# Kernel tuning notes

Measured on AMD Instinct MI355X. Metric: run time of the kernel, lower is better.

The kernel has to match this reference:

```python
import jax, jax.numpy as jnp
import numpy as np

B, C, W, H = 4, 128, 64, 64
CK = 32  # f/g projection channels


def setup_inputs() -> dict:
    key = jax.random.key(0)
    ks = jax.random.split(key, 8)
    s_in = 1.0 / np.sqrt(C)
    return {
        "x": jax.random.normal(ks[0], (B, C, W, H), dtype=jnp.float32),
        "Wf": jax.random.normal(ks[1], (CK, C), dtype=jnp.float32) * s_in,
        "bf": jnp.zeros((CK,), dtype=jnp.float32),
        "Wg": jax.random.normal(ks[2], (CK, C), dtype=jnp.float32) * s_in,
        "bg": jnp.zeros((CK,), dtype=jnp.float32),
        "Wh": jax.random.normal(ks[3], (C, C), dtype=jnp.float32) * s_in,
        "bh": jnp.zeros((C,), dtype=jnp.float32),
        "gamma": jax.random.normal(ks[4], (1,), dtype=jnp.float32) * 0.1,
    }


def reference(x, Wf, bf, Wg, bg, Wh, bh, gamma):
    b, c, w, h = x.shape
    n = w * h
    xf = x.reshape(b, c, n)                                  # [B,C,N]
    # 1x1 convs == per-pixel linear projections
    f = jnp.einsum('oc,bcn->bon', Wf, xf) + bf[None, :, None]  # [B,32,N]
    g = jnp.einsum('oc,bcn->bon', Wg, xf) + bg[None, :, None]  # [B,32,N]
    v = jnp.einsum('oc,bcn->bon', Wh, xf) + bh[None, :, None]  # [B,C,N]
    # attention = softmax(f^T g) over last dim (g positions), as in the torch code
    att = jax.nn.softmax(jnp.einsum('bkn,bkm->bnm', f, g), axis=-1)  # [B,N,N]
    # self_attention = h @ attention  (contract over f-position axis)
    sa = jnp.einsum('bcn,bnm->bcm', v, att).reshape(b, c, w, h)
    return gamma[0] * sa + x
```

## Files before the change

### kernel.cpp

```cpp
#include <hip/hip_runtime.h>
#include <hip/hip_bf16.h>

#define BB 4
#define CC 128
#define NN 4096
#define CK 32
#define L2E 1.442695040888963f

typedef __attribute__((ext_vector_type(8))) short short8v;
typedef __attribute__((ext_vector_type(4))) float float4v;

__device__ inline ushort f2bf(float f) {
    union { __hip_bfloat16 h; ushort u; } cv;
    cv.h = __float2bfloat16(f);
    return cv.u;
}
__device__ inline float bf2f(ushort u) {
    union { uint u; float f; } cv;
    cv.u = ((uint)u) << 16;
    return cv.f;
}
__device__ inline uint pk2(float lo, float hi) {
    return ((uint)f2bf(lo)) | ((uint)f2bf(hi) << 16);
}
__device__ __forceinline__ void gll16(const void* g, void* l) {
    __builtin_amdgcn_global_load_lds(
        (const __attribute__((address_space(1))) void*)g,
        (__attribute__((address_space(3))) void*)l, 16, 0, 0);
}

__global__ __launch_bounds__(512) void wprep_kernel(
    const float* __restrict__ Wf, const float* __restrict__ bf,
    const float* __restrict__ Wg, const float* __restrict__ bg,
    const float* __restrict__ Wh, const float* __restrict__ bh,
    const float* __restrict__ gamma,
    ushort* __restrict__ Wcat, float* __restrict__ bias_cat)
{
    const float sgn = (gamma[0] < 0.f) ? -1.f : 1.f;
    const int t = blockIdx.x * 512 + threadIdx.x;
    const int o = t >> 7, c = t & 127;
    float w, scale;
    if (o < 32)      { w = Wf[o * 128 + c];        scale = L2E;  }
    else if (o < 64) { w = Wg[(o - 32) * 128 + c]; scale = 1.f;  }
    else             { w = Wh[(o - 64) * 128 + c]; scale = sgn;  }
    Wcat[t] = f2bf(w * scale);
    if (t < 192) {
        const float bv = (t < 32) ? bf[t] * L2E
                       : (t < 64) ? bg[t - 32]
                                  : bh[t - 64] * sgn;
        bias_cat[t] = bv;
    }
}

__global__ __launch_bounds__(512) void proj_kernel(
    const float* __restrict__ x, const ushort* __restrict__ Wcat,
    const float* __restrict__ bias_cat,
    ushort* __restrict__ ft, ushort* __restrict__ gt, ushort* __restrict__ vh)
{
    __shared__ ushort xs[32][132];
    const int t  = threadIdx.x;
    const int n0 = blockIdx.x * 32;
    const int b  = blockIdx.y;
    const float* xb = x + (size_t)b * CC * NN;

    {
        const int nl = t & 31, cg = t >> 5;
        #pragma unroll
        for (int i = 0; i < 8; ++i) {
            const int c = cg + 16 * i;
            xs[nl][c] = f2bf(xb[(size_t)c * NN + n0 + nl]);
        }
    }
    __syncthreads();

    const int w   = t >> 6;
    const int l   = t & 63;
    const int g16 = l >> 4;
    const int l16 = l & 15;
    const int og  = w >> 1;
    const int nh  = w & 1;

    const float4v zf = {0.f, 0.f, 0.f, 0.f};
    float4v acc[3];
    #pragma unroll
    for (int tt = 0; tt < 3; ++tt) acc[tt] = zf;

    #pragma unroll
    for (int kt = 0; kt < 4; ++kt) {
        const short8v bfr = *reinterpret_cast<const short8v*>(
            &xs[nh * 16 + l16][32 * kt + 8 * g16]);
        #pragma unroll
        for (int tt = 0; tt < 3; ++tt) {
            const short8v afr = *reinterpret_cast<const short8v*>(
                &Wcat[(size_t)(48 * og + 16 * tt + l16) * 128 + 32 * kt + 8 * g16]);
            acc[tt] = __builtin_amdgcn_mfma_f32_16x16x32_bf16(afr, bfr, acc[tt], 0, 0, 0);
        }
    }

    const int n = n0 + nh * 16 + l16;
    #pragma unroll
    for (int tt = 0; tt < 3; ++tt) {
        const int ob = 48 * og + 16 * tt + 4 * g16;
        const float4 b4 = *reinterpret_cast<const float4*>(&bias_cat[ob]);
        const float v0 = acc[tt][0] + b4.x;
        const float v1 = acc[tt][1] + b4.y;
        const float v2 = acc[tt][2] + b4.z;
        const float v3 = acc[tt][3] + b4.w;
        if (ob < 32) {
            ushort4 pk;
            pk.x = f2bf(v0); pk.y = f2bf(v1); pk.z = f2bf(v2); pk.w = f2bf(v3);
            *reinterpret_cast<ushort4*>(&ft[((size_t)b * NN + n) * CK + ob]) = pk;
        } else if (ob < 64) {
            ushort4 pk;
            pk.x = f2bf(v0); pk.y = f2bf(v1); pk.z = f2bf(v2); pk.w = f2bf(v3);
            *reinterpret_cast<ushort4*>(&gt[((size_t)b * NN + n) * CK + (ob - 32)]) = pk;
        } else {
            const int c = ob - 64;
            vh[((size_t)b * CC + c + 0) * NN + n] = f2bf(v0);
            vh[((size_t)b * CC + c + 1) * NN + n] = f2bf(v1);
            vh[((size_t)b * CC + c + 2) * NN + n] = f2bf(v2);
            vh[((size_t)b * CC + c + 3) * NN + n] = f2bf(v3);
        }
    }
}

__global__ __launch_bounds__(256) void pass1_kernel(
    const ushort* __restrict__ ft, const ushort* __restrict__ gt,
    float* __restrict__ Dpart)
{
    const int t   = threadIdx.x;
    const int w   = t >> 6;
    const int l   = t & 63;
    const int g16 = l >> 4;
    const int l16 = l & 15;
    const int n0  = blockIdx.x * 64;
    const int b   = blockIdx.y;
    const int mz  = blockIdx.z;

    const ushort* ftb = ft + (size_t)b * NN * CK;
    const ushort* gtb = gt + (size_t)b * NN * CK;

    const short8v afrag = *reinterpret_cast<const short8v*>(
        &ftb[(size_t)(n0 + 16 * w + l16) * CK + 8 * g16]);

    const float4v zf = {0.f, 0.f, 0.f, 0.f};
    float d0 = 0.f, d1 = 0.f, d2 = 0.f, d3 = 0.f;
    const int m0 = mz * 512;

    short8v bfA = *reinterpret_cast<const short8v*>(
        &gtb[(size_t)(m0 + l16) * CK + 8 * g16]);
    #pragma unroll 1
    for (int mt = 0; mt < 32; mt += 2) {
        const short8v bfB = *reinterpret_cast<const short8v*>(
            &gtb[(size_t)(m0 + (mt + 1) * 16 + l16) * CK + 8 * g16]);
        float4v s = __builtin_amdgcn_mfma_f32_16x16x32_bf16(afrag, bfA, zf, 0, 0, 0);
        d0 += __builtin_amdgcn_exp2f(s[0]); d1 += __builtin_amdgcn_exp2f(s[1]);
        d2 += __builtin_amdgcn_exp2f(s[2]); d3 += __builtin_amdgcn_exp2f(s[3]);
        bfA = *reinterpret_cast<const short8v*>(
            &gtb[(size_t)(m0 + (((mt + 2) & 31)) * 16 + l16) * CK + 8 * g16]);
        float4v s2 = __builtin_amdgcn_mfma_f32_16x16x32_bf16(afrag, bfB, zf, 0, 0, 0);
        d0 += __builtin_amdgcn_exp2f(s2[0]); d1 += __builtin_amdgcn_exp2f(s2[1]);
        d2 += __builtin_amdgcn_exp2f(s2[2]); d3 += __builtin_amdgcn_exp2f(s2[3]);
    }
    #pragma unroll
    for (int msk = 1; msk <= 8; msk <<= 1) {
        d0 += __shfl_xor(d0, msk);
        d1 += __shfl_xor(d1, msk);
        d2 += __shfl_xor(d2, msk);
        d3 += __shfl_xor(d3, msk);
    }
    if (l16 < 4) {
        const int n = n0 + 16 * w + 4 * g16 + l16;
        const float v = (l16 == 0) ? d0 : (l16 == 1) ? d1 : (l16 == 2) ? d2 : d3;
        Dpart[((size_t)b * NN + n) * 8 + mz] = v;
    }
}

__global__ __launch_bounds__(256) void reduce_kernel(
    const float* __restrict__ Dpart, float* __restrict__ sc,
    const float* __restrict__ gamma)
{
    const int i = blockIdx.x * 256 + threadIdx.x;
    const float4 a4 = *reinterpret_cast<const float4*>(&Dpart[(size_t)i * 8]);
    const float4 b4 = *reinterpret_cast<const float4*>(&Dpart[(size_t)i * 8 + 4]);
    const float D = (a4.x + a4.y + a4.z + a4.w) + (b4.x + b4.y + b4.z + b4.w);
    sc[i] = fabsf(gamma[0]) / D;
}

__global__ __launch_bounds__(256) void vscale_kernel(
    ushort* __restrict__ vh, const float* __restrict__ sc)
{
    const size_t i8   = (size_t)blockIdx.x * 256 + threadIdx.x;
    const size_t base = i8 * 8;
    const int    n    = (int)(base & (NN - 1));
    const int    b    = (int)(base / ((size_t)CC * NN));

    ushort4 v0 = *reinterpret_cast<const ushort4*>(&vh[base]);
    ushort4 v1 = *reinterpret_cast<const ushort4*>(&vh[base + 4]);
    const float4 s0 = *reinterpret_cast<const float4*>(&sc[(size_t)b * NN + n]);
    const float4 s1 = *reinterpret_cast<const float4*>(&sc[(size_t)b * NN + n + 4]);

    v0.x = f2bf(bf2f(v0.x) * s0.x);
    v0.y = f2bf(bf2f(v0.y) * s0.y);
    v0.z = f2bf(bf2f(v0.z) * s0.z);
    v0.w = f2bf(bf2f(v0.w) * s0.w);
    v1.x = f2bf(bf2f(v1.x) * s1.x);
    v1.y = f2bf(bf2f(v1.y) * s1.y);
    v1.z = f2bf(bf2f(v1.z) * s1.z);
    v1.w = f2bf(bf2f(v1.w) * s1.w);

    *reinterpret_cast<ushort4*>(&vh[base])     = v0;
    *reinterpret_cast<ushort4*>(&vh[base + 4]) = v1;
}

#define WSTR  8192
#define VBUF  4096

__global__ __launch_bounds__(1024) void pass2_kernel(
    const ushort* __restrict__ ft, const ushort* __restrict__ gt,
    const ushort* __restrict__ vh,
    const float* __restrict__ x, float* __restrict__ out)
{
    __shared__ __align__(16) char smem[16 * WSTR];

    const int t   = threadIdx.x;
    const int w   = t >> 6;
    const int l   = t & 63;
    const int g16 = l >> 4;
    const int l16 = l & 15;
    const int ch  = w & 1;
    const int nq  = w >> 1;

    const int bid = blockIdx.x;
    const int xcd = bid & 7;
    const int b   = xcd >> 1;
    const int m0  = ((bid >> 3) + 32 * (xcd & 1)) * 64;

    const ushort* ftb = ft + (size_t)b * NN * CK;
    const ushort* gtb = gt + (size_t)b * NN * CK;
    const ushort* vhb = vh + (size_t)b * CC * NN;

    char* wsm = smem + w * WSTR;

    short8v gfrag[4];
    #pragma unroll
    for (int tm = 0; tm < 4; ++tm)
        gfrag[tm] = *reinterpret_cast<const short8v*>(
            &gtb[(size_t)(m0 + 16 * tm + l16) * CK + 8 * g16]);

    const float4v zf = {0.f, 0.f, 0.f, 0.f};
    float4v acc[4][4];
    #pragma unroll
    for (int tc = 0; tc < 4; ++tc)
        #pragma unroll
        for (int tm = 0; tm < 4; ++tm) acc[tc][tm] = zf;

    const int nbase = nq * 512;
    const int rr = l >> 2, cp = l & 3;

#define STAGE(n0_, bo_) do {                                                   \
    _Pragma("unroll")                                                          \
    for (int j = 0; j < 4; ++j) {                                              \
        const int row = j * 16 + rr;                                           \
        gll16(vhb + (size_t)(64 * ch + row) * NN + (n0_)                       \
                  + (((2 * cp) ^ (row & 6)) << 2),                             \
              wsm + (bo_) + j * 1024);                                         \
    }                                                                          \
} while (0)

    STAGE(nbase, 0);
    asm volatile("s_waitcnt vmcnt(0)" ::: "memory");

    int bo = 0;
    #pragma unroll 1
    for (int st = 0; st < 16; ++st) {
        const int n0 = nbase + st * 32;

        const short8v af0 = *reinterpret_cast<const short8v*>(
            &ftb[(size_t)(n0 + l16) * CK + 8 * g16]);
        const short8v af1 = *reinterpret_cast<const short8v*>(
            &ftb[(size_t)(n0 + 16 + l16) * CK + 8 * g16]);

        if (st < 15) {
            STAGE(n0 + 32, bo ^ VBUF);
            asm volatile("s_waitcnt vmcnt(4)" ::: "memory");
        } else {
            asm volatile("s_waitcnt vmcnt(0)" ::: "memory");
        }

        const char* Vb = wsm + bo;

        union { uint u[4]; short8v s; } pf[4];
        #pragma unroll
        for (int tm = 0; tm < 4; ++tm) {
            float4v s0 = __builtin_amdgcn_mfma_f32_16x16x32_bf16(af0, gfrag[tm], zf, 0, 0, 0);
            float4v s1 = __builtin_amdgcn_mfma_f32_16x16x32_bf16(af1, gfrag[tm], zf, 0, 0, 0);
            pf[tm].u[0] = pk2(__builtin_amdgcn_exp2f(s0[0]), __builtin_amdgcn_exp2f(s0[1]));
            pf[tm].u[1] = pk2(__builtin_amdgcn_exp2f(s0[2]), __builtin_amdgcn_exp2f(s0[3]));
            pf[tm].u[2] = pk2(__builtin_amdgcn_exp2f(s1[0]), __builtin_amdgcn_exp2f(s1[1]));
            pf[tm].u[3] = pk2(__builtin_amdgcn_exp2f(s1[2]), __builtin_amdgcn_exp2f(s1[3]));
        }

        #pragma unroll
        for (int tc = 0; tc < 4; ++tc) {
            const int cl = 16 * tc + l16;
            const uint2 va  = *reinterpret_cast<const uint2*>(
                Vb + cl * 64 + 8 * (g16 ^ (cl & 6)));
            const uint2 vb2 = *reinterpret_cast<const uint2*>(
                Vb + cl * 64 + 8 * ((4 + g16) ^ (cl & 6)));
            union { uint u[4]; short8v s; } av;
            av.u[0] = va.x;  av.u[1] = va.y;
            av.u[2] = vb2.x; av.u[3] = vb2.y;
            #pragma unroll
            for (int tm = 0; tm < 4; ++tm)
                acc[tc][tm] = __builtin_amdgcn_mfma_f32_16x16x32_bf16(av.s, pf[tm].s, acc[tc][tm], 0, 0, 0);
        }
        bo ^= VBUF;
    }
#undef STAGE

    float4v* rl = (float4v*)smem;
    __syncthreads();
    if (nq >= 4) {
        const int slot = (nq - 4) * 2 + ch;
        #pragma unroll
        for (int tc = 0; tc < 4; ++tc)
            #pragma unroll
            for (int tm = 0; tm < 4; ++tm)
                rl[(slot * 16 + tc * 4 + tm) * 64 + l] = acc[tc][tm];
    }
    __syncthreads();
    if (nq < 4) {
        const int slot = nq * 2 + ch;
        #pragma unroll
        for (int tc = 0; tc < 4; ++tc)
            #pragma unroll
            for (int tm = 0; tm < 4; ++tm)
                acc[tc][tm] += rl[(slot * 16 + tc * 4 + tm) * 64 + l];
    }
    __syncthreads();
    if (nq == 2 || nq == 3) {
        const int slot = (nq - 2) * 2 + ch;
        #pragma unroll
        for (int tc = 0; tc < 4; ++tc)
            #pragma unroll
            for (int tm = 0; tm < 4; ++tm)
                rl[(slot * 16 + tc * 4 + tm) * 64 + l] = acc[tc][tm];
    }
    __syncthreads();
    if (nq < 2) {
        const int slot = nq * 2 + ch;
        #pragma unroll
        for (int tc = 0; tc < 4; ++tc)
            #pragma unroll
            for (int tm = 0; tm < 4; ++tm)
                acc[tc][tm] += rl[(slot * 16 + tc * 4 + tm) * 64 + l];
    }
    __syncthreads();
    if (nq == 1) {
        #pragma unroll
        for (int tc = 0; tc < 4; ++tc)
            #pragma unroll
            for (int tm = 0; tm < 4; ++tm)
                rl[(ch * 16 + tc * 4 + tm) * 64 + l] = acc[tc][tm];
    }
    __syncthreads();
    if (nq == 0) {
        const float* xb = x   + (size_t)b * CC * NN;
        float*       ob = out + (size_t)b * CC * NN;
        #pragma unroll
        for (int tc = 0; tc < 4; ++tc) {
            #pragma unroll
            for (int tm = 0; tm < 4; ++tm) {
                float4v s = acc[tc][tm] + rl[(ch * 16 + tc * 4 + tm) * 64 + l];
                const int cb = 64 * ch + 16 * tc + 4 * g16;
                const int m  = m0 + 16 * tm + l16;
                #pragma unroll
                for (int r = 0; r < 4; ++r) {
                    const size_t idx = (size_t)(cb + r) * NN + m;
                    ob[idx] = s[r] + xb[idx];
                }
            }
        }
    }
}

extern "C" void kernel_launch(void* const* d_in, const int* in_sizes, int n_in,
                              void* d_out, int out_size, void* d_ws, size_t ws_size,
                              hipStream_t stream)
{
    const float* x     = (const float*)d_in[0];
    const float* Wf    = (const float*)d_in[1];
    const float* bf    = (const float*)d_in[2];
    const float* Wg    = (const float*)d_in[3];
    const float* bg    = (const float*)d_in[4];
    const float* Wh    = (const float*)d_in[5];
    const float* bh    = (const float*)d_in[6];
    const float* gamma = (const float*)d_in[7];

    ushort* ft = (ushort*)d_ws;
    ushort* gt = ft + (size_t)BB * NN * CK;
    ushort* vh = gt + (size_t)BB * NN * CK;
    float* Dpart = (float*)(vh + (size_t)BB * CC * NN);
    float* sc    = Dpart + (size_t)BB * NN * 8;
    float* bias_cat = sc + (size_t)BB * NN;
    ushort* Wcat = (ushort*)(bias_cat + 192);

    float* out = (float*)d_out;

    wprep_kernel<<<dim3(48), 512, 0, stream>>>(Wf, bf, Wg, bg, Wh, bh, gamma, Wcat, bias_cat);
    proj_kernel<<<dim3(NN / 32, BB), 512, 0, stream>>>(x, Wcat, bias_cat, ft, gt, vh);
    pass1_kernel<<<dim3(NN / 64, BB, 8), 256, 0, stream>>>(ft, gt, Dpart);
    reduce_kernel<<<dim3(BB * NN / 256), 256, 0, stream>>>(Dpart, sc, gamma);
    vscale_kernel<<<dim3(BB * CC * NN / 8 / 256), 256, 0, stream>>>(vh, sc);
    pass2_kernel<<<dim3(256), 1024, 0, stream>>>(ft, gt, vh, x, out);
}
```

Measured before the change: 82.50 us.

## Fold softmax row scaling into pass2 and retile to smaller blocks with prefetch

Removes the separate vscale kernel and instead multiplies each exp2 score by the per-row scale sc inside pass2. This saves a full read-modify-write pass over vh. pass2 is retiled to 512-thread blocks covering 32 output columns each, with 512 blocks and 4 n-partitions per channel half, so the cross-wave reduction shrinks to a single LDS step. The f fragments and scale values for the next step are now prefetched with inline-asm loads alongside the LDS staging. The cost is extra VALU multiplies and more redundant V streaming per output column, since each block covers fewer columns.

```diff
diff --git a/kernel.cpp b/kernel.cpp
--- a/kernel.cpp
+++ b/kernel.cpp
@@ -15,11 +15,6 @@
     cv.h = __float2bfloat16(f);
     return cv.u;
 }
-__device__ inline float bf2f(ushort u) {
-    union { uint u; float f; } cv;
-    cv.u = ((uint)u) << 16;
-    return cv.f;
-}
 __device__ inline uint pk2(float lo, float hi) {
     return ((uint)f2bf(lo)) | ((uint)f2bf(hi) << 16);
 }
@@ -27,6 +22,18 @@
     __builtin_amdgcn_global_load_lds(
         (const __attribute__((address_space(1))) void*)g,
         (__attribute__((address_space(3))) void*)l, 16, 0, 0);
+}
+__device__ __forceinline__ short8v gload16(const ushort* addr) {
+    short8v r;
+    asm volatile("global_load_dwordx4 %0, %1, off"
+                 : "=v"(r) : "v"(addr) : "memory");
+    return r;
+}
+__device__ __forceinline__ float4v gload16f(const float* addr) {
+    float4v r;
+    asm volatile("global_load_dwordx4 %0, %1, off"
+                 : "=v"(r) : "v"(addr) : "memory");
+    return r;
 }
 
 __global__ __launch_bounds__(512) void wprep_kernel(
@@ -187,41 +194,15 @@
     sc[i] = fabsf(gamma[0]) / D;
 }
 
-__global__ __launch_bounds__(256) void vscale_kernel(
-    ushort* __restrict__ vh, const float* __restrict__ sc)
-{
-    const size_t i8   = (size_t)blockIdx.x * 256 + threadIdx.x;
-    const size_t base = i8 * 8;
-    const int    n    = (int)(base & (NN - 1));
-    const int    b    = (int)(base / ((size_t)CC * NN));
-
-    ushort4 v0 = *reinterpret_cast<const ushort4*>(&vh[base]);
-    ushort4 v1 = *reinterpret_cast<const ushort4*>(&vh[base + 4]);
-    const float4 s0 = *reinterpret_cast<const float4*>(&sc[(size_t)b * NN + n]);
-    const float4 s1 = *reinterpret_cast<const float4*>(&sc[(size_t)b * NN + n + 4]);
-
-    v0.x = f2bf(bf2f(v0.x) * s0.x);
-    v0.y = f2bf(bf2f(v0.y) * s0.y);
-    v0.z = f2bf(bf2f(v0.z) * s0.z);
-    v0.w = f2bf(bf2f(v0.w) * s0.w);
-    v1.x = f2bf(bf2f(v1.x) * s1.x);
-    v1.y = f2bf(bf2f(v1.y) * s1.y);
-    v1.z = f2bf(bf2f(v1.z) * s1.z);
-    v1.w = f2bf(bf2f(v1.w) * s1.w);
-
-    *reinterpret_cast<ushort4*>(&vh[base])     = v0;
-    *reinterpret_cast<ushort4*>(&vh[base + 4]) = v1;
-}
-
 #define WSTR  8192
 #define VBUF  4096
 
-__global__ __launch_bounds__(1024) void pass2_kernel(
+__global__ __launch_bounds__(512, 4) void pass2_kernel(
     const ushort* __restrict__ ft, const ushort* __restrict__ gt,
-    const ushort* __restrict__ vh,
+    const ushort* __restrict__ vh, const float* __restrict__ sc,
     const float* __restrict__ x, float* __restrict__ out)
 {
-    __shared__ __align__(16) char smem[16 * WSTR];
+    __shared__ __align__(16) char smem[8 * WSTR];
 
     const int t   = threadIdx.x;
     const int w   = t >> 6;
@@ -234,29 +215,32 @@
     const int bid = blockIdx.x;
     const int xcd = bid & 7;
     const int b   = xcd >> 1;
-    const int m0  = ((bid >> 3) + 32 * (xcd & 1)) * 64;
+    const int m0  = ((bid >> 3) + 64 * (xcd & 1)) * 32;
 
     const ushort* ftb = ft + (size_t)b * NN * CK;
     const ushort* gtb = gt + (size_t)b * NN * CK;
     const ushort* vhb = vh + (size_t)b * CC * NN;
+    const float*  scb = sc + (size_t)b * NN;
 
     char* wsm = smem + w * WSTR;
 
-    short8v gfrag[4];
-    #pragma unroll
-    for (int tm = 0; tm < 4; ++tm)
+    short8v gfrag[2];
+    #pragma unroll
+    for (int tm = 0; tm < 2; ++tm)
         gfrag[tm] = *reinterpret_cast<const short8v*>(
             &gtb[(size_t)(m0 + 16 * tm + l16) * CK + 8 * g16]);
 
     const float4v zf = {0.f, 0.f, 0.f, 0.f};
-    float4v acc[4][4];
+    float4v acc[4][2];
     #pragma unroll
     for (int tc = 0; tc < 4; ++tc)
         #pragma unroll
-        for (int tm = 0; tm < 4; ++tm) acc[tc][tm] = zf;
-
-    const int nbase = nq * 512;
+        for (int tm = 0; tm < 2; ++tm) acc[tc][tm] = zf;
+
+    const int nbase = nq * 1024;
     const int rr = l >> 2, cp = l & 3;
+    const ushort* afp = ftb + (size_t)l16 * CK + 8 * g16;
+    const float*  scp = scb + 4 * g16;
 
 #define STAGE(n0_, bo_) do {                                                   \
     _Pragma("unroll")                                                          \
@@ -269,36 +253,39 @@
 } while (0)
 
     STAGE(nbase, 0);
+    short8v afA0 = gload16(afp + (size_t)nbase * CK);
+    short8v afA1 = gload16(afp + (size_t)(nbase + 16) * CK);
+    float4v scA0 = gload16f(scp + nbase);
+    float4v scA1 = gload16f(scp + nbase + 16);
     asm volatile("s_waitcnt vmcnt(0)" ::: "memory");
 
     int bo = 0;
     #pragma unroll 1
-    for (int st = 0; st < 16; ++st) {
-        const int n0 = nbase + st * 32;
-
-        const short8v af0 = *reinterpret_cast<const short8v*>(
-            &ftb[(size_t)(n0 + l16) * CK + 8 * g16]);
-        const short8v af1 = *reinterpret_cast<const short8v*>(
-            &ftb[(size_t)(n0 + 16 + l16) * CK + 8 * g16]);
-
-        if (st < 15) {
-            STAGE(n0 + 32, bo ^ VBUF);
-            asm volatile("s_waitcnt vmcnt(4)" ::: "memory");
-        } else {
-            asm volatile("s_waitcnt vmcnt(0)" ::: "memory");
-        }
+    for (int st = 0; st < 32; ++st) {
+        const int n1 = nbase + ((st + 1) & 31) * 32;
+
+        STAGE(n1, bo ^ VBUF);
+        short8v afB0 = gload16(afp + (size_t)n1 * CK);
+        short8v afB1 = gload16(afp + (size_t)(n1 + 16) * CK);
+        float4v scB0 = gload16f(scp + n1);
+        float4v scB1 = gload16f(scp + n1 + 16);
+        asm volatile("s_waitcnt vmcnt(8)" ::: "memory");
 
         const char* Vb = wsm + bo;
 
-        union { uint u[4]; short8v s; } pf[4];
-        #pragma unroll
-        for (int tm = 0; tm < 4; ++tm) {
-            float4v s0 = __builtin_amdgcn_mfma_f32_16x16x32_bf16(af0, gfrag[tm], zf, 0, 0, 0);
-            float4v s1 = __builtin_amdgcn_mfma_f32_16x16x32_bf16(af1, gfrag[tm], zf, 0, 0, 0);
-            pf[tm].u[0] = pk2(__builtin_amdgcn_exp2f(s0[0]), __builtin_amdgcn_exp2f(s0[1]));
-            pf[tm].u[1] = pk2(__builtin_amdgcn_exp2f(s0[2]), __builtin_amdgcn_exp2f(s0[3]));
-            pf[tm].u[2] = pk2(__builtin_amdgcn_exp2f(s1[0]), __builtin_amdgcn_exp2f(s1[1]));
-            pf[tm].u[3] = pk2(__builtin_amdgcn_exp2f(s1[2]), __builtin_amdgcn_exp2f(s1[3]));
+        union { uint u[4]; short8v s; } pf[2];
+        #pragma unroll
+        for (int tm = 0; tm < 2; ++tm) {
+            float4v s0 = __builtin_amdgcn_mfma_f32_16x16x32_bf16(afA0, gfrag[tm], zf, 0, 0, 0);
+            float4v s1 = __builtin_amdgcn_mfma_f32_16x16x32_bf16(afA1, gfrag[tm], zf, 0, 0, 0);
+            pf[tm].u[0] = pk2(__builtin_amdgcn_exp2f(s0[0]) * scA0[0],
+                              __builtin_amdgcn_exp2f(s0[1]) * scA0[1]);
+            pf[tm].u[1] = pk2(__builtin_amdgcn_exp2f(s0[2]) * scA0[2],
+                              __builtin_amdgcn_exp2f(s0[3]) * scA0[3]);
+            pf[tm].u[2] = pk2(__builtin_amdgcn_exp2f(s1[0]) * scA1[0],
+                              __builtin_amdgcn_exp2f(s1[1]) * scA1[1]);
+            pf[tm].u[3] = pk2(__builtin_amdgcn_exp2f(s1[2]) * scA1[2],
+                              __builtin_amdgcn_exp2f(s1[3]) * scA1[3]);
         }
 
         #pragma unroll
@@ -311,58 +298,25 @@
             union { uint u[4]; short8v s; } av;
             av.u[0] = va.x;  av.u[1] = va.y;
             av.u[2] = vb2.x; av.u[3] = vb2.y;
-            #pragma unroll
-            for (int tm = 0; tm < 4; ++tm)
-                acc[tc][tm] = __builtin_amdgcn_mfma_f32_16x16x32_bf16(av.s, pf[tm].s, acc[tc][tm], 0, 0, 0);
-        }
+            acc[tc][0] = __builtin_amdgcn_mfma_f32_16x16x32_bf16(av.s, pf[0].s, acc[tc][0], 0, 0, 0);
+            acc[tc][1] = __builtin_amdgcn_mfma_f32_16x16x32_bf16(av.s, pf[1].s, acc[tc][1], 0, 0, 0);
+        }
+
+        afA0 = afB0; afA1 = afB1;
+        scA0 = scB0; scA1 = scB1;
         bo ^= VBUF;
     }
 #undef STAGE
 
+    __syncthreads();
     float4v* rl = (float4v*)smem;
-    __syncthreads();
-    if (nq >= 4) {
-        const int slot = (nq - 4) * 2 + ch;
+    if (nq != 0) {
+        const int slot = (nq - 1) * 2 + ch;
         #pragma unroll
         for (int tc = 0; tc < 4; ++tc)
             #pragma unroll
-            for (int tm = 0; tm < 4; ++tm)
-                rl[(slot * 16 + tc * 4 + tm) * 64 + l] = acc[tc][tm];
-    }
-    __syncthreads();
-    if (nq < 4) {
-        const int slot = nq * 2 + ch;
-        #pragma unroll
-        for (int tc = 0; tc < 4; ++tc)
-            #pragma unroll
-            for (int tm = 0; tm < 4; ++tm)
-                acc[tc][tm] += rl[(slot * 16 + tc * 4 + tm) * 64 + l];
-    }
-    __syncthreads();
-    if (nq == 2 || nq == 3) {
-        const int slot = (nq - 2) * 2 + ch;
-        #pragma unroll
-        for (int tc = 0; tc < 4; ++tc)
-            #pragma unroll
-            for (int tm = 0; tm < 4; ++tm)
-                rl[(slot * 16 + tc * 4 + tm) * 64 + l] = acc[tc][tm];
-    }
-    __syncthreads();
-    if (nq < 2) {
-        const int slot = nq * 2 + ch;
-        #pragma unroll
-        for (int tc = 0; tc < 4; ++tc)
-            #pragma unroll
-            for (int tm = 0; tm < 4; ++tm)
-                acc[tc][tm] += rl[(slot * 16 + tc * 4 + tm) * 64 + l];
-    }
-    __syncthreads();
-    if (nq == 1) {
-        #pragma unroll
-        for (int tc = 0; tc < 4; ++tc)
-            #pragma unroll
-            for (int tm = 0; tm < 4; ++tm)
-                rl[(ch * 16 + tc * 4 + tm) * 64 + l] = acc[tc][tm];
+            for (int tm = 0; tm < 2; ++tm)
+                rl[(slot * 8 + tc * 2 + tm) * 64 + l] = acc[tc][tm];
     }
     __syncthreads();
     if (nq == 0) {
@@ -371,8 +325,12 @@
         #pragma unroll
         for (int tc = 0; tc < 4; ++tc) {
             #pragma unroll
-            for (int tm = 0; tm < 4; ++tm) {
-                float4v s = acc[tc][tm] + rl[(ch * 16 + tc * 4 + tm) * 64 + l];
+            for (int tm = 0; tm < 2; ++tm) {
+                const int fi = tc * 2 + tm;
+                float4v s = acc[tc][tm]
+                          + rl[((ch) * 8 + fi) * 64 + l]
+                          + rl[((2 + ch) * 8 + fi) * 64 + l]
+                          + rl[((4 + ch) * 8 + fi) * 64 + l];
                 const int cb = 64 * ch + 16 * tc + 4 * g16;
                 const int m  = m0 + 16 * tm + l16;
                 #pragma unroll
@@ -412,6 +370,5 @@
     proj_kernel<<<dim3(NN / 32, BB), 512, 0, stream>>>(x, Wcat, bias_cat, ft, gt, vh);
     pass1_kernel<<<dim3(NN / 64, BB, 8), 256, 0, stream>>>(ft, gt, Dpart);
     reduce_kernel<<<dim3(BB * NN / 256), 256, 0, stream>>>(Dpart, sc, gamma);
-    vscale_kernel<<<dim3(BB * CC * NN / 8 / 256), 256, 0, stream>>>(vh, sc);
-    pass2_kernel<<<dim3(256), 1024, 0, stream>>>(ft, gt, vh, x, out);
-}
+    pass2_kernel<<<dim3(512), 512, 0, stream>>>(ft, gt, vh, sc, x, out);
+}
```

Result: slower. 92.18 us (+11.7%).
